# Kernel optimization log

Hardware: AMD Instinct MI355X
Metric: run time of the kernel (lower is better)

The kernel has to match this reference:

```python
import jax, jax.numpy as jnp
import numpy as np

N_ATOMS = 500000
N_BONDS = 1000000
MAX_NB = 6
ATOM_FDIM = 133
BOND_FDIM = 14
HIDDEN = 128
MP_DEPTH = 3
ATOMS_PER_MOL = 20


def setup_inputs() -> dict:
    key = jax.random.key(0)
    ks = jax.random.split(key, 12)
    inp = {
        "f_atoms": jax.random.normal(ks[0], (N_ATOMS, ATOM_FDIM), jnp.float32),
        "f_bonds": jax.random.normal(ks[1], (N_BONDS, BOND_FDIM), jnp.float32),
        "Wi_w": jax.random.normal(ks[2], (HIDDEN, ATOM_FDIM), jnp.float32) * 0.05,
        "Wi_b": jax.random.normal(ks[3], (HIDDEN,), jnp.float32) * 0.05,
        "Wh_w": jax.random.normal(ks[4], (HIDDEN, HIDDEN + BOND_FDIM), jnp.float32) * 0.05,
        "Wh_b": jax.random.normal(ks[5], (HIDDEN,), jnp.float32) * 0.05,
        "Wo_w": jax.random.normal(ks[6], (HIDDEN, ATOM_FDIM + HIDDEN), jnp.float32) * 0.05,
        "Wo_b": jax.random.normal(ks[7], (HIDDEN,), jnp.float32) * 0.05,
        "ffn_w": jax.random.normal(ks[8], (1, HIDDEN), jnp.float32) * 0.05,
        "ffn_b": jax.random.normal(ks[9], (1,), jnp.float32) * 0.05,
        "a2a": jax.random.randint(ks[10], (N_ATOMS, MAX_NB), 0, N_ATOMS, jnp.int32),
        "a2b": jax.random.randint(ks[11], (N_ATOMS, MAX_NB), 0, N_BONDS, jnp.int32),
        "atoms_per_mol": ATOMS_PER_MOL,
    }
    return inp


def reference(f_atoms, f_bonds, Wi_w, Wi_b, Wh_w, Wh_b, Wo_w, Wo_b, ffn_w, ffn_b,
              a2a, a2b, atoms_per_mol):
    # W_i + ReLU: initial atom messages
    x = f_atoms @ Wi_w.T + Wi_b                     # [N_atoms, H]
    message = jax.nn.relu(x)
    # pre-aggregate bond features once (constant across depths)
    nei_f_bonds_sum = f_bonds[a2b].sum(axis=1)      # [N_atoms, BOND_FDIM]
    for _ in range(MP_DEPTH - 1):
        # gather neighbor messages and sum (index_select_ND + sum(dim=1));
        # concat(msg_gather, bond_gather).sum(1) == concat(sum(msg), sum(bond))
        nei_a_message = message[a2a].sum(axis=1)    # [N_atoms, H]
        nei = jnp.concatenate([nei_a_message, nei_f_bonds_sum], axis=1)
        message = jax.nn.relu(x + nei @ Wh_w.T + Wh_b)
        # dropout is identity in eval mode
    # final aggregation + W_o
    a_message = message[a2a].sum(axis=1)            # [N_atoms, H]
    a_input = jnp.concatenate([f_atoms, a_message], axis=1)
    atom_hiddens = jax.nn.relu(a_input @ Wo_w.T + Wo_b)
    # max readout per molecule (equal-size a_scope of atoms_per_mol)
    n_atoms, h = atom_hiddens.shape
    mol_vecs = atom_hiddens.reshape(n_atoms // atoms_per_mol, atoms_per_mol, h).max(axis=1)
    # FFN head (NN_depth=1): Dropout (identity) + Linear(H -> 1)
    return mol_vecs @ ffn_w.T + ffn_b               # [n_mols, 1]
```

## Files before the change

kernel.cpp:

```cpp
#include <hip/hip_runtime.h>
#include <hip/hip_bf16.h>

#define N_ATOMS   500000
#define N_BONDS   1000000
#define MAX_NB    6
#define ATOM_FDIM 133
#define BOND_FDIM 14
#define HIDDEN    128
#define N_MOLS    25000
#define APM       20

typedef __attribute__((ext_vector_type(8))) short short8;
typedef __attribute__((ext_vector_type(4))) float f32x4;
typedef unsigned short u16;
typedef unsigned int   u32;

__device__ __forceinline__ float bf2f(u16 u) {
    u32 t = ((u32)u) << 16;
    return __builtin_bit_cast(float, t);
}
__device__ __forceinline__ u16 f2bf(float f) {
    u32 t = __builtin_bit_cast(u32, f);
    t += 0x7FFFu + ((t >> 16) & 1u);
    return (u16)(t >> 16);
}

__global__ void prep_weights(const float* __restrict__ Wi, const float* __restrict__ Wh,
                             const float* __restrict__ Wo,
                             u16* __restrict__ Wip, u16* __restrict__ Whp, u16* __restrict__ Wop) {
    int stride = gridDim.x * blockDim.x;
    int tid = blockIdx.x * blockDim.x + threadIdx.x;
    for (int i = tid; i < 128 * 160; i += stride) {
        int r = i / 160, c = i % 160;
        Wip[i] = (c < 133) ? f2bf(Wi[r * 133 + c]) : (u16)0;
        Whp[i] = (c < 142) ? f2bf(Wh[r * 142 + c]) : (u16)0;
    }
    for (int i = tid; i < 128 * 288; i += stride) {
        int r = i / 288, c = i % 288;
        float v = 0.f;
        if (c < 133)      v = Wo[r * 261 + c];
        else if (c >= 160) v = Wo[r * 261 + (c - 27)];
        Wop[i] = f2bf(v);
    }
}

#define CROWS 24
__global__ __launch_bounds__(256) void fa_convert(const float* __restrict__ fa, u16* __restrict__ out) {
    __shared__ float buf[CROWS * 133];
    const long row0 = (long)blockIdx.x * CROWS;
    const int rows = (int)((N_ATOMS - row0) < CROWS ? (N_ATOMS - row0) : CROWS);
    const float* src = fa + row0 * ATOM_FDIM;
    if (rows == CROWS) {
        for (int i = threadIdx.x; i < (CROWS * 133) / 4; i += 256)
            *(float4*)(&buf[i * 4]) = *(const float4*)(src + i * 4);
    } else {
        for (int i = threadIdx.x; i < rows * 133; i += 256) buf[i] = src[i];
    }
    __syncthreads();
    for (int j = threadIdx.x; j < rows * 20; j += 256) {
        int r = j / 20, c8 = (j % 20) * 8;
        u16 u[8];
#pragma unroll
        for (int e = 0; e < 8; e++) {
            int c = c8 + e;
            u[e] = (c < ATOM_FDIM) ? f2bf(buf[r * 133 + c]) : (u16)0;
        }
        uint4 v;
        v.x = (u32)u[0] | ((u32)u[1] << 16);
        v.y = (u32)u[2] | ((u32)u[3] << 16);
        v.z = (u32)u[4] | ((u32)u[5] << 16);
        v.w = (u32)u[6] | ((u32)u[7] << 16);
        *(uint4*)(out + (row0 + r) * 160 + c8) = v;
    }
}

__global__ __launch_bounds__(256) void bond_gather(const float* __restrict__ fb, const int* __restrict__ a2b,
                                                   u16* __restrict__ outp) {
    long t = (long)blockIdx.x * 256 + threadIdx.x;
    int atom = (int)(t >> 4);
    int c2   = (int)(t & 15);
    if (atom >= N_ATOMS) return;
    int c0 = 2 * c2, c1 = c0 + 1;
    float s0 = 0.f, s1 = 0.f;
    if (c0 < BOND_FDIM) {
#pragma unroll
        for (int j = 0; j < MAX_NB; j++) {
            int idx = a2b[atom * 6 + j];
            const float* row = fb + (long)idx * BOND_FDIM;
            s0 += row[c0];
            if (c1 < BOND_FDIM) s1 += row[c1];
        }
    }
    *(u32*)(outp + (long)atom * 32 + c0) = (u32)f2bf(s0) | ((u32)f2bf(s1) << 16);
}

__global__ __launch_bounds__(256) void gather_relu_sum(const u16* __restrict__ src,
                                                       const int* __restrict__ a2a,
                                                       u16* __restrict__ dst) {
    long t = (long)blockIdx.x * 256 + threadIdx.x;
    int atom = (int)(t >> 4);
    int c8   = (int)(t & 15) << 3;
    float s[8] = {0, 0, 0, 0, 0, 0, 0, 0};
#pragma unroll
    for (int j = 0; j < MAX_NB; j++) {
        int idx = a2a[atom * 6 + j];
        uint4 v = *(const uint4*)(src + (long)idx * 128 + c8);
        u32 w[4] = {v.x, v.y, v.z, v.w};
#pragma unroll
        for (int q = 0; q < 4; q++) {
            s[2 * q]     += fmaxf(__builtin_bit_cast(float, w[q] << 16), 0.f);
            s[2 * q + 1] += fmaxf(__builtin_bit_cast(float, w[q] & 0xFFFF0000u), 0.f);
        }
    }
    uint4 o;
    o.x = (u32)f2bf(s[0]) | ((u32)f2bf(s[1]) << 16);
    o.y = (u32)f2bf(s[2]) | ((u32)f2bf(s[3]) << 16);
    o.z = (u32)f2bf(s[4]) | ((u32)f2bf(s[5]) << 16);
    o.w = (u32)f2bf(s[6]) | ((u32)f2bf(s[7]) << 16);
    *(uint4*)(dst + (long)atom * 128 + c8) = o;
}

template <int KB0, int KB1, bool ADDX>
__global__ __launch_bounds__(256, 2) void gemm_mp(
    const u16* __restrict__ A0, int ldA0,
    const u16* __restrict__ A1, int ldA1,
    const u16* __restrict__ Wp, const float* __restrict__ bias,
    const u16* __restrict__ Xadd, u16* __restrict__ Out) {
    constexpr int KB  = KB0 + KB1;
    constexpr int KP  = KB * 32;
    constexpr int LDW = KP + 8;
    __shared__ u16 ldsw[128 * LDW];

    const int lane = threadIdx.x & 63;
    const int wave = threadIdx.x >> 6;
    const int lrow = lane & 15;
    const int kg   = lane >> 4;
    const long rowbase = (long)blockIdx.x * 128 + wave * 32;

    long ar[2];
#pragma unroll
    for (int m = 0; m < 2; m++) {
        long r = rowbase + m * 16 + lrow;
        if (r >= N_ATOMS) r = N_ATOMS - 1;
        ar[m] = r;
    }

    uint4 a0v[2][KB0 ? KB0 : 1];
    uint4 a1v[2][KB1 ? KB1 : 1];
#pragma unroll
    for (int m = 0; m < 2; m++) {
        if constexpr (KB0 > 0) {
            const u16* p0 = A0 + ar[m] * ldA0 + kg * 8;
#pragma unroll
            for (int kb = 0; kb < KB0; kb++) a0v[m][kb] = *(const uint4*)(p0 + kb * 32);
        }
        if constexpr (KB1 > 0) {
            const u16* p1 = A1 + ar[m] * ldA1 + kg * 8;
#pragma unroll
            for (int kb = 0; kb < KB1; kb++) a1v[m][kb] = *(const uint4*)(p1 + kb * 32);
        }
    }
    uint2 xv[2][8];
    if constexpr (ADDX) {
#pragma unroll
        for (int m = 0; m < 2; m++) {
#pragma unroll
            for (int n = 0; n < 8; n++)
                xv[m][n] = *(const uint2*)(Xadd + ar[m] * 128 + n * 16 + kg * 4);
        }
    }

    for (int i = threadIdx.x; i < 128 * (KP / 8); i += 256) {
        int r  = i / (KP / 8);
        int c8 = (i % (KP / 8)) * 8;
        *(uint4*)(&ldsw[r * LDW + c8]) = *(const uint4*)(Wp + r * KP + c8);
    }
    __syncthreads();

    f32x4 acc[2][8];
#pragma unroll
    for (int m = 0; m < 2; m++)
#pragma unroll
        for (int n = 0; n < 8; n++) acc[m][n] = (f32x4){0.f, 0.f, 0.f, 0.f};

#pragma unroll
    for (int kb = 0; kb < KB; kb++) {
        short8 af[2];
#pragma unroll
        for (int m = 0; m < 2; m++) {
            if (kb < KB0) af[m] = __builtin_bit_cast(short8, a0v[m][kb < KB0 ? kb : 0]);
            else          af[m] = __builtin_bit_cast(short8, a1v[m][(kb - KB0) < KB1 ? (kb - KB0) : 0]);
        }
#pragma unroll
        for (int n = 0; n < 8; n++) {
            short8 bf = __builtin_bit_cast(short8, *(const uint4*)(&ldsw[(n * 16 + lrow) * LDW + kb * 32 + kg * 8]));
            acc[0][n] = __builtin_amdgcn_mfma_f32_16x16x32_bf16(bf, af[0], acc[0][n], 0, 0, 0);
            acc[1][n] = __builtin_amdgcn_mfma_f32_16x16x32_bf16(bf, af[1], acc[1][n], 0, 0, 0);
        }
    }

#pragma unroll
    for (int m = 0; m < 2; m++) {
        long r = rowbase + m * 16 + lrow;
        if (r >= N_ATOMS) continue;
#pragma unroll
        for (int n = 0; n < 8; n++) {
            int c0 = n * 16 + kg * 4;
            float4 b4 = *(const float4*)(bias + c0);
            float v0 = acc[m][n][0] + b4.x;
            float v1 = acc[m][n][1] + b4.y;
            float v2 = acc[m][n][2] + b4.z;
            float v3 = acc[m][n][3] + b4.w;
            if constexpr (ADDX) {
                v0 += __builtin_bit_cast(float, xv[m][n].x << 16);
                v1 += __builtin_bit_cast(float, xv[m][n].x & 0xFFFF0000u);
                v2 += __builtin_bit_cast(float, xv[m][n].y << 16);
                v3 += __builtin_bit_cast(float, xv[m][n].y & 0xFFFF0000u);
            }
            uint2 o;
            o.x = (u32)f2bf(v0) | ((u32)f2bf(v1) << 16);
            o.y = (u32)f2bf(v2) | ((u32)f2bf(v3) << 16);
            *(uint2*)(Out + r * 128 + c0) = o;
        }
    }
}

__global__ __launch_bounds__(256) void readout(const u16* __restrict__ ah,
                                               const float* __restrict__ ffn_w,
                                               const float* __restrict__ ffn_b,
                                               float* __restrict__ out) {
    int mol  = blockIdx.x * 4 + (threadIdx.x >> 6);
    int lane = threadIdx.x & 63;
    if (mol >= N_MOLS) return;
    float m0 = -1e30f, m1 = -1e30f;
    const u16* base = ah + (long)mol * APM * 128 + 2 * lane;
#pragma unroll
    for (int a = 0; a < APM; a++) {
        u32 v = *(const u32*)(base + a * 128);
        m0 = fmaxf(m0, bf2f((u16)(v & 0xFFFFu)));
        m1 = fmaxf(m1, bf2f((u16)(v >> 16)));
    }
    m0 = fmaxf(m0, 0.f);
    m1 = fmaxf(m1, 0.f);
    float p = m0 * ffn_w[2 * lane] + m1 * ffn_w[2 * lane + 1];
#pragma unroll
    for (int off = 32; off > 0; off >>= 1) p += __shfl_down(p, off);
    if (lane == 0) out[mol] = p + ffn_b[0];
}

extern "C" void kernel_launch(void* const* d_in, const int* in_sizes, int n_in,
                              void* d_out, int out_size, void* d_ws, size_t ws_size,
                              hipStream_t stream) {
    const float* f_atoms = (const float*)d_in[0];
    const float* f_bonds = (const float*)d_in[1];
    const float* Wi_w = (const float*)d_in[2];
    const float* Wi_b = (const float*)d_in[3];
    const float* Wh_w = (const float*)d_in[4];
    const float* Wh_b = (const float*)d_in[5];
    const float* Wo_w = (const float*)d_in[6];
    const float* Wo_b = (const float*)d_in[7];
    const float* ffn_w = (const float*)d_in[8];
    const float* ffn_b = (const float*)d_in[9];
    const int* a2a = (const int*)d_in[10];
    const int* a2b = (const int*)d_in[11];
    float* out = (float*)d_out;

    char* ws = (char*)d_ws;
    u16* fa    = (u16*)(ws);
    u16* xb    = (u16*)(ws + 160000000L);
    u16* msgA  = (u16*)(ws + 288000000L);
    u16* msgB  = (u16*)(ws + 416000000L);
    u16* nsum  = (u16*)(ws + 544000000L);
    u16* nbond = (u16*)(ws + 672000000L);
    u16* Wip   = (u16*)(ws + 704000000L);
    u16* Whp   = (u16*)(ws + 704040960L);
    u16* Wop   = (u16*)(ws + 704081920L);

    prep_weights<<<64, 256, 0, stream>>>(Wi_w, Wh_w, Wo_w, Wip, Whp, Wop);
    fa_convert<<<(N_ATOMS + CROWS - 1) / CROWS, 256, 0, stream>>>(f_atoms, fa);
    bond_gather<<<31250, 256, 0, stream>>>(f_bonds, a2b, nbond);

    gemm_mp<5, 0, false><<<3907, 256, 0, stream>>>(
        fa, 160, (const u16*)nullptr, 0, Wip, Wi_b, (const u16*)nullptr, xb);

    gather_relu_sum<<<31250, 256, 0, stream>>>(xb, a2a, nsum);
    gemm_mp<4, 1, true><<<3907, 256, 0, stream>>>(
        nsum, 128, nbond, 32, Whp, Wh_b, xb, msgA);
    gather_relu_sum<<<31250, 256, 0, stream>>>(msgA, a2a, nsum);
    gemm_mp<4, 1, true><<<3907, 256, 0, stream>>>(
        nsum, 128, nbond, 32, Whp, Wh_b, xb, msgB);
    gather_relu_sum<<<31250, 256, 0, stream>>>(msgB, a2a, nsum);
    gemm_mp<5, 4, false><<<3907, 256, 0, stream>>>(
        fa, 160, nsum, 128, Wop, Wo_b, (const u16*)nullptr, msgA);

    readout<<<6250, 256, 0, stream>>>(msgA, ffn_w, ffn_b, out);
}
```

Baseline: 1.017 ms.

## Split GEMM output columns across two blocks to raise occupancy

Each gemm_mp block now computes only half of the 128 output columns, selected by the low bit of blockIdx. The grid doubles, the LDS weight tile and accumulator array halve, and launch bounds request 4 blocks per SM. The X-add operand is loaded in the epilogue instead of being prefetched. In exchange, each A-row tile is read twice from global memory, and the LDS row padding is removed, which may cause bank conflicts on the B-fragment reads.

```diff
diff --git a/kernel.cpp b/kernel.cpp
--- a/kernel.cpp
+++ b/kernel.cpp
@@ -121,21 +121,22 @@
 }
 
 template <int KB0, int KB1, bool ADDX>
-__global__ __launch_bounds__(256, 2) void gemm_mp(
+__global__ __launch_bounds__(256, 4) void gemm_mp(
     const u16* __restrict__ A0, int ldA0,
     const u16* __restrict__ A1, int ldA1,
     const u16* __restrict__ Wp, const float* __restrict__ bias,
     const u16* __restrict__ Xadd, u16* __restrict__ Out) {
-    constexpr int KB  = KB0 + KB1;
-    constexpr int KP  = KB * 32;
-    constexpr int LDW = KP + 8;
-    __shared__ u16 ldsw[128 * LDW];
-
+    constexpr int KB = KB0 + KB1;
+    constexpr int KP = KB * 32;
+    __shared__ u16 ldsw[64 * KP];
+
+    const int nh   = blockIdx.x & 1;
+    const int mblk = blockIdx.x >> 1;
     const int lane = threadIdx.x & 63;
     const int wave = threadIdx.x >> 6;
     const int lrow = lane & 15;
     const int kg   = lane >> 4;
-    const long rowbase = (long)blockIdx.x * 128 + wave * 32;
+    const long rowbase = (long)mblk * 128 + wave * 32;
 
     long ar[2];
 #pragma unroll
@@ -160,28 +161,20 @@
             for (int kb = 0; kb < KB1; kb++) a1v[m][kb] = *(const uint4*)(p1 + kb * 32);
         }
     }
-    uint2 xv[2][8];
-    if constexpr (ADDX) {
-#pragma unroll
-        for (int m = 0; m < 2; m++) {
-#pragma unroll
-            for (int n = 0; n < 8; n++)
-                xv[m][n] = *(const uint2*)(Xadd + ar[m] * 128 + n * 16 + kg * 4);
-        }
-    }
-
-    for (int i = threadIdx.x; i < 128 * (KP / 8); i += 256) {
-        int r  = i / (KP / 8);
-        int c8 = (i % (KP / 8)) * 8;
-        *(uint4*)(&ldsw[r * LDW + c8]) = *(const uint4*)(Wp + r * KP + c8);
+
+    {
+        const u16* wsrc = Wp + (size_t)nh * 64 * KP;
+        constexpr int TOT8 = 64 * KP / 8;
+        for (int f = threadIdx.x; f < TOT8; f += 256)
+            *(uint4*)(&ldsw[f * 8]) = *(const uint4*)(wsrc + f * 8);
     }
     __syncthreads();
 
-    f32x4 acc[2][8];
+    f32x4 acc[2][4];
 #pragma unroll
     for (int m = 0; m < 2; m++)
 #pragma unroll
-        for (int n = 0; n < 8; n++) acc[m][n] = (f32x4){0.f, 0.f, 0.f, 0.f};
+        for (int n = 0; n < 4; n++) acc[m][n] = (f32x4){0.f, 0.f, 0.f, 0.f};
 
 #pragma unroll
     for (int kb = 0; kb < KB; kb++) {
@@ -192,8 +185,8 @@
             else          af[m] = __builtin_bit_cast(short8, a1v[m][(kb - KB0) < KB1 ? (kb - KB0) : 0]);
         }
 #pragma unroll
-        for (int n = 0; n < 8; n++) {
-            short8 bf = __builtin_bit_cast(short8, *(const uint4*)(&ldsw[(n * 16 + lrow) * LDW + kb * 32 + kg * 8]));
+        for (int n = 0; n < 4; n++) {
+            short8 bf = __builtin_bit_cast(short8, *(const uint4*)(&ldsw[(n * 16 + lrow) * KP + kb * 32 + kg * 8]));
             acc[0][n] = __builtin_amdgcn_mfma_f32_16x16x32_bf16(bf, af[0], acc[0][n], 0, 0, 0);
             acc[1][n] = __builtin_amdgcn_mfma_f32_16x16x32_bf16(bf, af[1], acc[1][n], 0, 0, 0);
         }
@@ -204,18 +197,19 @@
         long r = rowbase + m * 16 + lrow;
         if (r >= N_ATOMS) continue;
 #pragma unroll
-        for (int n = 0; n < 8; n++) {
-            int c0 = n * 16 + kg * 4;
+        for (int n = 0; n < 4; n++) {
+            int c0 = nh * 64 + n * 16 + kg * 4;
             float4 b4 = *(const float4*)(bias + c0);
             float v0 = acc[m][n][0] + b4.x;
             float v1 = acc[m][n][1] + b4.y;
             float v2 = acc[m][n][2] + b4.z;
             float v3 = acc[m][n][3] + b4.w;
             if constexpr (ADDX) {
-                v0 += __builtin_bit_cast(float, xv[m][n].x << 16);
-                v1 += __builtin_bit_cast(float, xv[m][n].x & 0xFFFF0000u);
-                v2 += __builtin_bit_cast(float, xv[m][n].y << 16);
-                v3 += __builtin_bit_cast(float, xv[m][n].y & 0xFFFF0000u);
+                uint2 xv = *(const uint2*)(Xadd + r * 128 + c0);
+                v0 += __builtin_bit_cast(float, xv.x << 16);
+                v1 += __builtin_bit_cast(float, xv.x & 0xFFFF0000u);
+                v2 += __builtin_bit_cast(float, xv.y << 16);
+                v3 += __builtin_bit_cast(float, xv.y & 0xFFFF0000u);
             }
             uint2 o;
             o.x = (u32)f2bf(v0) | ((u32)f2bf(v1) << 16);
@@ -280,17 +274,17 @@
     fa_convert<<<(N_ATOMS + CROWS - 1) / CROWS, 256, 0, stream>>>(f_atoms, fa);
     bond_gather<<<31250, 256, 0, stream>>>(f_bonds, a2b, nbond);
 
-    gemm_mp<5, 0, false><<<3907, 256, 0, stream>>>(
+    gemm_mp<5, 0, false><<<7814, 256, 0, stream>>>(
         fa, 160, (const u16*)nullptr, 0, Wip, Wi_b, (const u16*)nullptr, xb);
 
     gather_relu_sum<<<31250, 256, 0, stream>>>(xb, a2a, nsum);
-    gemm_mp<4, 1, true><<<3907, 256, 0, stream>>>(
+    gemm_mp<4, 1, true><<<7814, 256, 0, stream>>>(
         nsum, 128, nbond, 32, Whp, Wh_b, xb, msgA);
     gather_relu_sum<<<31250, 256, 0, stream>>>(msgA, a2a, nsum);
-    gemm_mp<4, 1, true><<<3907, 256, 0, stream>>>(
+    gemm_mp<4, 1, true><<<7814, 256, 0, stream>>>(
         nsum, 128, nbond, 32, Whp, Wh_b, xb, msgB);
     gather_relu_sum<<<31250, 256, 0, stream>>>(msgB, a2a, nsum);
-    gemm_mp<5, 4, false><<<3907, 256, 0, stream>>>(
+    gemm_mp<5, 4, false><<<7814, 256, 0, stream>>>(
         fa, 160, nsum, 128, Wop, Wo_b, (const u16*)nullptr, msgA);
 
     readout<<<6250, 256, 0, stream>>>(msgA, ffn_w, ffn_b, out);
```

Result: no change. 1.018 ms (+0.0%).

## Make GEMM kernels persistent with double-buffered global-to-LDS async loads

Applied to the files above, without the earlier changes.

Replaces the one-tile-per-block GEMM with a persistent kernel that loops over 16-row-per-wave tiles. It loads weights into LDS once per block using direct global-to-LDS loads, then double-buffers the A operand and residual X tiles so the next tile's loads overlap the current tile's MFMAs. This is meant to cut the repeated per-block weight loading and hide memory latency. In exchange each wave now owns 16 rows instead of 32, the grids shrink to a few hundred blocks, and correctness leans on the exact vmcnt wait counts and the LDS layout matching the MFMA fragment ordering.

```diff
diff --git a/kernel.cpp b/kernel.cpp
--- a/kernel.cpp
+++ b/kernel.cpp
@@ -23,6 +23,12 @@
     u32 t = __builtin_bit_cast(u32, f);
     t += 0x7FFFu + ((t >> 16) & 1u);
     return (u16)(t >> 16);
+}
+
+__device__ __forceinline__ void gl16(const u16* g, u16* l) {
+    __builtin_amdgcn_global_load_lds(
+        (__attribute__((address_space(1))) void*)(g),
+        (__attribute__((address_space(3))) void*)(l), 16, 0, 0);
 }
 
 __global__ void prep_weights(const float* __restrict__ Wi, const float* __restrict__ Wh,
@@ -120,108 +126,117 @@
     *(uint4*)(dst + (long)atom * 128 + c8) = o;
 }
 
-template <int KB0, int KB1, bool ADDX>
-__global__ __launch_bounds__(256, 2) void gemm_mp(
+template <int KB0, int KB1, bool ADDX, int WAVES>
+__global__ __launch_bounds__(WAVES * 64, 2) void gemm_pp(
     const u16* __restrict__ A0, int ldA0,
     const u16* __restrict__ A1, int ldA1,
     const u16* __restrict__ Wp, const float* __restrict__ bias,
     const u16* __restrict__ Xadd, u16* __restrict__ Out) {
-    constexpr int KB  = KB0 + KB1;
-    constexpr int KP  = KB * 32;
-    constexpr int LDW = KP + 8;
-    __shared__ u16 ldsw[128 * LDW];
+    constexpr int KB   = KB0 + KB1;
+    constexpr int KP   = KB * 32;
+    constexpr int TILE = WAVES * 16;
+    constexpr long NT  = (N_ATOMS + TILE - 1) / TILE;
+    constexpr int WSLOTS = KB * 8;
+    constexpr int ASLOTS = 2 * WAVES * KB;
+    constexpr int XSLOTS = ADDX ? 2 * WAVES * 4 : 0;
+    constexpr int NVM  = KB + (ADDX ? 4 : 0);
+    __shared__ __align__(16) u16 lds[(WSLOTS + ASLOTS + XSLOTS) * 512];
 
     const int lane = threadIdx.x & 63;
     const int wave = threadIdx.x >> 6;
     const int lrow = lane & 15;
     const int kg   = lane >> 4;
-    const long rowbase = (long)blockIdx.x * 128 + wave * 32;
-
-    long ar[2];
-#pragma unroll
-    for (int m = 0; m < 2; m++) {
-        long r = rowbase + m * 16 + lrow;
+
+    u16* WL = lds;
+    u16* AL = lds + WSLOTS * 512;
+    u16* XL = lds + (WSLOTS + ASLOTS) * 512;
+
+    for (int s = wave; s < WSLOTS; s += WAVES) {
+        int kb = s >> 3, n = s & 7;
+        gl16(Wp + (n * 16 + lrow) * KP + kb * 32 + kg * 8, WL + s * 512);
+    }
+    asm volatile("s_waitcnt vmcnt(0)" ::: "memory");
+    __syncthreads();
+
+    float4 b4[8];
+#pragma unroll
+    for (int n = 0; n < 8; n++) b4[n] = *(const float4*)(bias + n * 16 + kg * 4);
+
+    const int G = gridDim.x;
+
+    auto stage = [&](int buf, long t) {
+        long row0w = t * TILE + wave * 16;
+        long r = row0w + lrow;
         if (r >= N_ATOMS) r = N_ATOMS - 1;
-        ar[m] = r;
-    }
-
-    uint4 a0v[2][KB0 ? KB0 : 1];
-    uint4 a1v[2][KB1 ? KB1 : 1];
-#pragma unroll
-    for (int m = 0; m < 2; m++) {
+        u16* ab = AL + (buf * WAVES + wave) * KB * 512;
         if constexpr (KB0 > 0) {
-            const u16* p0 = A0 + ar[m] * ldA0 + kg * 8;
-#pragma unroll
-            for (int kb = 0; kb < KB0; kb++) a0v[m][kb] = *(const uint4*)(p0 + kb * 32);
+            const u16* p = A0 + r * ldA0 + kg * 8;
+#pragma unroll
+            for (int kb = 0; kb < KB0; kb++) gl16(p + kb * 32, ab + kb * 512);
         }
         if constexpr (KB1 > 0) {
-            const u16* p1 = A1 + ar[m] * ldA1 + kg * 8;
-#pragma unroll
-            for (int kb = 0; kb < KB1; kb++) a1v[m][kb] = *(const uint4*)(p1 + kb * 32);
-        }
-    }
-    uint2 xv[2][8];
-    if constexpr (ADDX) {
-#pragma unroll
-        for (int m = 0; m < 2; m++) {
-#pragma unroll
-            for (int n = 0; n < 8; n++)
-                xv[m][n] = *(const uint2*)(Xadd + ar[m] * 128 + n * 16 + kg * 4);
-        }
-    }
-
-    for (int i = threadIdx.x; i < 128 * (KP / 8); i += 256) {
-        int r  = i / (KP / 8);
-        int c8 = (i % (KP / 8)) * 8;
-        *(uint4*)(&ldsw[r * LDW + c8]) = *(const uint4*)(Wp + r * KP + c8);
-    }
-    __syncthreads();
-
-    f32x4 acc[2][8];
-#pragma unroll
-    for (int m = 0; m < 2; m++)
-#pragma unroll
-        for (int n = 0; n < 8; n++) acc[m][n] = (f32x4){0.f, 0.f, 0.f, 0.f};
-
-#pragma unroll
-    for (int kb = 0; kb < KB; kb++) {
-        short8 af[2];
-#pragma unroll
-        for (int m = 0; m < 2; m++) {
-            if (kb < KB0) af[m] = __builtin_bit_cast(short8, a0v[m][kb < KB0 ? kb : 0]);
-            else          af[m] = __builtin_bit_cast(short8, a1v[m][(kb - KB0) < KB1 ? (kb - KB0) : 0]);
-        }
-#pragma unroll
-        for (int n = 0; n < 8; n++) {
-            short8 bf = __builtin_bit_cast(short8, *(const uint4*)(&ldsw[(n * 16 + lrow) * LDW + kb * 32 + kg * 8]));
-            acc[0][n] = __builtin_amdgcn_mfma_f32_16x16x32_bf16(bf, af[0], acc[0][n], 0, 0, 0);
-            acc[1][n] = __builtin_amdgcn_mfma_f32_16x16x32_bf16(bf, af[1], acc[1][n], 0, 0, 0);
-        }
-    }
-
-#pragma unroll
-    for (int m = 0; m < 2; m++) {
-        long r = rowbase + m * 16 + lrow;
-        if (r >= N_ATOMS) continue;
-#pragma unroll
-        for (int n = 0; n < 8; n++) {
-            int c0 = n * 16 + kg * 4;
-            float4 b4 = *(const float4*)(bias + c0);
-            float v0 = acc[m][n][0] + b4.x;
-            float v1 = acc[m][n][1] + b4.y;
-            float v2 = acc[m][n][2] + b4.z;
-            float v3 = acc[m][n][3] + b4.w;
-            if constexpr (ADDX) {
-                v0 += __builtin_bit_cast(float, xv[m][n].x << 16);
-                v1 += __builtin_bit_cast(float, xv[m][n].x & 0xFFFF0000u);
-                v2 += __builtin_bit_cast(float, xv[m][n].y << 16);
-                v3 += __builtin_bit_cast(float, xv[m][n].y & 0xFFFF0000u);
+            const u16* p = A1 + r * ldA1 + kg * 8;
+#pragma unroll
+            for (int kb = 0; kb < KB1; kb++) gl16(p + kb * 32, ab + (KB0 + kb) * 512);
+        }
+        if constexpr (ADDX) {
+            u16* xbse = XL + (buf * WAVES + wave) * 4 * 512;
+#pragma unroll
+            for (int j = 0; j < 4; j++) {
+                long rx = row0w + j * 4 + (lane >> 4);
+                if (rx >= N_ATOMS) rx = N_ATOMS - 1;
+                gl16(Xadd + rx * 128 + (lane & 15) * 8, xbse + j * 512);
             }
-            uint2 o;
-            o.x = (u32)f2bf(v0) | ((u32)f2bf(v1) << 16);
-            o.y = (u32)f2bf(v2) | ((u32)f2bf(v3) << 16);
-            *(uint2*)(Out + r * 128 + c0) = o;
-        }
+        }
+    };
+
+    int buf = 0;
+    long t0 = blockIdx.x;
+    stage(0, t0);
+    for (long t = t0; t < NT; t += G) {
+        long tn = (t + G < NT) ? (t + G) : t;
+        stage(buf ^ 1, tn);
+        asm volatile("s_waitcnt vmcnt(%0)" :: "n"(NVM) : "memory");
+        __builtin_amdgcn_sched_barrier(0);
+
+        const u16* abase = AL + (buf * WAVES + wave) * KB * 512;
+        f32x4 acc[8];
+#pragma unroll
+        for (int n = 0; n < 8; n++) acc[n] = (f32x4){0.f, 0.f, 0.f, 0.f};
+#pragma unroll
+        for (int kb = 0; kb < KB; kb++) {
+            short8 af = *(const short8*)(abase + kb * 512 + lane * 8);
+#pragma unroll
+            for (int n = 0; n < 8; n++) {
+                short8 bf = *(const short8*)(WL + (kb * 8 + n) * 512 + lane * 8);
+                acc[n] = __builtin_amdgcn_mfma_f32_16x16x32_bf16(bf, af, acc[n], 0, 0, 0);
+            }
+        }
+
+        long r = t * TILE + wave * 16 + lrow;
+        if (r < N_ATOMS) {
+            const u16* xbse = XL + (buf * WAVES + wave) * 4 * 512 +
+                              (lrow >> 2) * 512 + (lrow & 3) * 128 + (kg >> 1) * 8 + (kg & 1) * 4;
+#pragma unroll
+            for (int n = 0; n < 8; n++) {
+                float v0 = acc[n][0] + b4[n].x;
+                float v1 = acc[n][1] + b4[n].y;
+                float v2 = acc[n][2] + b4[n].z;
+                float v3 = acc[n][3] + b4[n].w;
+                if constexpr (ADDX) {
+                    uint2 xr = *(const uint2*)(xbse + n * 16);
+                    v0 += __builtin_bit_cast(float, xr.x << 16);
+                    v1 += __builtin_bit_cast(float, xr.x & 0xFFFF0000u);
+                    v2 += __builtin_bit_cast(float, xr.y << 16);
+                    v3 += __builtin_bit_cast(float, xr.y & 0xFFFF0000u);
+                }
+                uint2 o;
+                o.x = (u32)f2bf(v0) | ((u32)f2bf(v1) << 16);
+                o.y = (u32)f2bf(v2) | ((u32)f2bf(v3) << 16);
+                *(uint2*)(Out + r * 128 + n * 16 + kg * 4) = o;
+            }
+        }
+        buf ^= 1;
     }
 }
 
@@ -280,17 +295,17 @@
     fa_convert<<<(N_ATOMS + CROWS - 1) / CROWS, 256, 0, stream>>>(f_atoms, fa);
     bond_gather<<<31250, 256, 0, stream>>>(f_bonds, a2b, nbond);
 
-    gemm_mp<5, 0, false><<<3907, 256, 0, stream>>>(
+    gemm_pp<5, 0, false, 4><<<512, 256, 0, stream>>>(
         fa, 160, (const u16*)nullptr, 0, Wip, Wi_b, (const u16*)nullptr, xb);
 
     gather_relu_sum<<<31250, 256, 0, stream>>>(xb, a2a, nsum);
-    gemm_mp<4, 1, true><<<3907, 256, 0, stream>>>(
+    gemm_pp<4, 1, true, 4><<<256, 256, 0, stream>>>(
         nsum, 128, nbond, 32, Whp, Wh_b, xb, msgA);
     gather_relu_sum<<<31250, 256, 0, stream>>>(msgA, a2a, nsum);
-    gemm_mp<4, 1, true><<<3907, 256, 0, stream>>>(
+    gemm_pp<4, 1, true, 4><<<256, 256, 0, stream>>>(
         nsum, 128, nbond, 32, Whp, Wh_b, xb, msgB);
     gather_relu_sum<<<31250, 256, 0, stream>>>(msgB, a2a, nsum);
-    gemm_mp<5, 4, false><<<3907, 256, 0, stream>>>(
+    gemm_pp<5, 4, false, 3><<<256, 192, 0, stream>>>(
         fa, 160, nsum, 128, Wop, Wo_b, (const u16*)nullptr, msgA);
 
     readout<<<6250, 256, 0, stream>>>(msgA, ffn_w, ffn_b, out);
```

Result: faster. 885.2 us (-13.0%).
